# Kernel tuning notes

Measured on AMD Instinct MI355X. Metric: run time of the kernel, lower is better.

Reference implementation:

```python
import jax, jax.numpy as jnp
import numpy as np

DIM = 512
HIDDEN = 1024
H2 = HIDDEN // 2
B = 384


def setup_inputs() -> dict:
    key = jax.random.key(0)
    ks = jax.random.split(key, 10)
    s_in = 1.0 / np.sqrt(DIM)
    s_h = 1.0 / np.sqrt(H2)
    return {
        "x_samples": jax.random.normal(ks[0], (B, DIM), dtype=jnp.float32),
        "y_samples": jax.random.normal(ks[1], (B, DIM), dtype=jnp.float32),
        "w1_mu": jax.random.uniform(ks[2], (DIM, H2), jnp.float32, -s_in, s_in),
        "b1_mu": jax.random.uniform(ks[3], (H2,), jnp.float32, -s_in, s_in),
        "w2_mu": jax.random.uniform(ks[4], (H2, DIM), jnp.float32, -s_h, s_h),
        "b2_mu": jax.random.uniform(ks[5], (DIM,), jnp.float32, -s_h, s_h),
        "w1_lv": jax.random.uniform(ks[6], (DIM, H2), jnp.float32, -s_in, s_in),
        "b1_lv": jax.random.uniform(ks[7], (H2,), jnp.float32, -s_in, s_in),
        "w2_lv": jax.random.uniform(ks[8], (H2, DIM), jnp.float32, -s_h, s_h),
        "b2_lv": jax.random.uniform(ks[9], (DIM,), jnp.float32, -s_h, s_h),
    }


def reference(x_samples, y_samples, w1_mu, b1_mu, w2_mu, b2_mu,
              w1_lv, b1_lv, w2_lv, b2_lv):
    batch_size = y_samples.shape[0]
    # p_mu / p_logvar MLPs
    mu = jax.nn.relu(x_samples @ w1_mu + b1_mu) @ w2_mu + b2_mu           # [B, D]
    logvar = jnp.tanh(jax.nn.relu(x_samples @ w1_lv + b1_lv) @ w2_lv + b2_lv)  # [B, D]
    inv_var = jnp.exp(-logvar)

    # positive log-likelihood per sample
    positive = (-(mu - y_samples) ** 2 * 0.5 * inv_var - logvar * 0.5).sum(-1)  # [B]

    # pairwise Gaussian log-likelihoods: all_probs[i, j] = log N(y_j; mu_i)
    diff = y_samples[None, :, :] - mu[:, None, :]                          # [B, B, D]
    all_probs = (-diff ** 2 * 0.5 * inv_var[:, None, :]
                 - logvar[:, None, :] * 0.5).sum(-1)                       # [B, B]

    # faithful to the torch broadcast: [B,B] + [B,B,1] -> [B,B,B]
    diag_mask = jnp.eye(batch_size, dtype=jnp.float32)[:, :, None] * -20.0  # [B, B, 1]
    scores = all_probs + diag_mask                                         # [B, B, B]
    negative = jax.scipy.special.logsumexp(scores, axis=0) - jnp.log(batch_size - 1.0)  # [B, B]

    upper = (positive - negative).mean()

    loglikeli = (-(mu - y_samples) ** 2 * inv_var - logvar).sum(1).mean(0)
    return loglikeli + jax.lax.stop_gradient(-loglikeli + upper)
```

## Files before the change

kernel.cpp:

```cpp
#include <hip/hip_runtime.h>
#include <math.h>

#define DIM  512
#define H2   512
#define BSZ  384



template<bool RELU>
__device__ __forceinline__ void gemm_tile(
    const float* __restrict__ A, const float* __restrict__ B,
    const float* __restrict__ bias, float* __restrict__ C,
    int m0, int n0,
    float (*As)[34], float (*Bs)[64])
{
    const int tid = threadIdx.x;
    const int tx = tid & 15;
    const int ty = tid >> 4;

    const int r_a  = tid >> 3;
    const int kg_a = tid & 7;
    const int kr_b = tid >> 4;
    const int cg_b = tid & 15;

    float acc[2][4] = {};

    float4 a_pf  = *(const float4*)&A[(size_t)(m0 + r_a) * 512 + kg_a * 4];
    float4 b_pf0 = *(const float4*)&B[(size_t)kr_b        * 512 + n0 + cg_b * 4];
    float4 b_pf1 = *(const float4*)&B[(size_t)(kr_b + 16) * 512 + n0 + cg_b * 4];

    for (int it = 0; it < 16; ++it) {
        __syncthreads();
        {
            float av[4];
            *(float4*)av = a_pf;
            #pragma unroll
            for (int j = 0; j < 4; ++j) As[kg_a * 4 + j][r_a] = av[j];
            *(float4*)&Bs[kr_b][cg_b * 4]      = b_pf0;
            *(float4*)&Bs[kr_b + 16][cg_b * 4] = b_pf1;
        }
        __syncthreads();

        if (it < 15) {
            const int k0n = (it + 1) * 32;
            a_pf  = *(const float4*)&A[(size_t)(m0 + r_a) * 512 + k0n + kg_a * 4];
            b_pf0 = *(const float4*)&B[(size_t)(k0n + kr_b)      * 512 + n0 + cg_b * 4];
            b_pf1 = *(const float4*)&B[(size_t)(k0n + kr_b + 16) * 512 + n0 + cg_b * 4];
        }

        #pragma unroll
        for (int kk = 0; kk < 32; ++kk) {
            const float a0 = As[kk][ty * 2 + 0];
            const float a1 = As[kk][ty * 2 + 1];
            const float4 bv = *(const float4*)&Bs[kk][tx * 4];
            acc[0][0] += a0 * bv.x; acc[0][1] += a0 * bv.y;
            acc[0][2] += a0 * bv.z; acc[0][3] += a0 * bv.w;
            acc[1][0] += a1 * bv.x; acc[1][1] += a1 * bv.y;
            acc[1][2] += a1 * bv.z; acc[1][3] += a1 * bv.w;
        }
    }

    float bb[4] = {0.f, 0.f, 0.f, 0.f};
    if (RELU) *(float4*)bb = *(const float4*)&bias[n0 + tx * 4];
    #pragma unroll
    for (int i = 0; i < 2; ++i) {
        float4 o;
        if (RELU) {
            o.x = fmaxf(acc[i][0] + bb[0], 0.f);
            o.y = fmaxf(acc[i][1] + bb[1], 0.f);
            o.z = fmaxf(acc[i][2] + bb[2], 0.f);
            o.w = fmaxf(acc[i][3] + bb[3], 0.f);
        } else {
            o.x = acc[i][0]; o.y = acc[i][1]; o.z = acc[i][2]; o.w = acc[i][3];
        }
        *(float4*)&C[(size_t)(m0 + ty * 2 + i) * 512 + n0 + tx * 4] = o;
    }
}

__global__ __launch_bounds__(256) void k_layer1(
    const float* __restrict__ x,
    const float* __restrict__ w1mu, const float* __restrict__ b1mu,
    const float* __restrict__ w1lv, const float* __restrict__ b1lv,
    const float* __restrict__ y,
    float* __restrict__ hmu, float* __restrict__ hlv,
    float* __restrict__ m1p, float* __restrict__ m2p)
{
    __shared__ float As[32][34];
    __shared__ float Bs[32][64];

    const int b = blockIdx.x;
    const int tid = threadIdx.x;

    if (b >= 192) {
        __shared__ float r1[2][512];
        __shared__ float r2[2][512];
        const int sb = b - 192;
        const int c4 = tid & 127;
        const int rh = tid >> 7;
        const int r0 = sb * 64 + rh * 32;
        float s1[4] = {0.f, 0.f, 0.f, 0.f};
        float s2[4] = {0.f, 0.f, 0.f, 0.f};
        for (int r = 0; r < 32; ++r) {
            float v[4];
            *(float4*)v = *(const float4*)&y[(size_t)(r0 + r) * 512 + c4 * 4];
            #pragma unroll
            for (int j = 0; j < 4; ++j) { s1[j] += v[j]; s2[j] += v[j] * v[j]; }
        }
        #pragma unroll
        for (int j = 0; j < 4; ++j) { r1[rh][c4 * 4 + j] = s1[j]; r2[rh][c4 * 4 + j] = s2[j]; }
        __syncthreads();
        if (rh == 0) {
            float4 o1, o2;
            o1.x = s1[0] + r1[1][c4 * 4 + 0]; o1.y = s1[1] + r1[1][c4 * 4 + 1];
            o1.z = s1[2] + r1[1][c4 * 4 + 2]; o1.w = s1[3] + r1[1][c4 * 4 + 3];
            o2.x = s2[0] + r2[1][c4 * 4 + 0]; o2.y = s2[1] + r2[1][c4 * 4 + 1];
            o2.z = s2[2] + r2[1][c4 * 4 + 2]; o2.w = s2[3] + r2[1][c4 * 4 + 3];
            *(float4*)&m1p[sb * 512 + c4 * 4] = o1;
            *(float4*)&m2p[sb * 512 + c4 * 4] = o2;
        }
        return;
    }

    const int branch = b >> 7 >= 1 ? 1 : (b >= 96 ? 1 : 0);
    const int idx = branch ? b - 96 : b;
    const int m0 = (idx >> 3) * 32;
    const int n0 = (idx & 7) * 64;

    if (branch == 0)
        gemm_tile<true>(x, w1mu, b1mu, hmu, m0, n0, As, Bs);
    else
        gemm_tile<true>(x, w1lv, b1lv, hlv, m0, n0, As, Bs);
}

__global__ __launch_bounds__(256) void k_layer2(
    const float* __restrict__ hmu, const float* __restrict__ hlv,
    const float* __restrict__ w2mu, const float* __restrict__ w2lv,
    float* __restrict__ gmu, float* __restrict__ glv)
{
    __shared__ float As[32][34];
    __shared__ float Bs[32][64];

    const int b = blockIdx.x;
    const int branch = b >= 96 ? 1 : 0;
    const int idx = branch ? b - 96 : b;
    const int m0 = (idx >> 3) * 32;
    const int n0 = (idx & 7) * 64;

    if (branch == 0)
        gemm_tile<false>(hmu, w2mu, nullptr, gmu, m0, n0, As, Bs);
    else
        gemm_tile<false>(hlv, w2lv, nullptr, glv, m0, n0, As, Bs);
}

__global__ __launch_bounds__(256) void k_epilogue(
    const float* __restrict__ gmu, const float* __restrict__ glv,
    const float* __restrict__ b2mu, const float* __restrict__ b2lv,
    const float* __restrict__ y,
    const float* __restrict__ m1p, const float* __restrict__ m2p,
    double* __restrict__ partials)
{
    __shared__ double wsum[4];
    const int tid = threadIdx.x;
    const float inv_b = 1.0f / (float)BSZ;

    float tsum = 0.f;
    #pragma unroll
    for (int jj = 0; jj < 2; ++jj) {
        const int e4 = blockIdx.x * 512 + tid * 2 + jj;
        const int col4 = e4 & 127;
        const size_t off = (size_t)e4 * 4;

        float gm[4], gl[4], yv[4], bm[4], bl[4], s1[4], s2[4];
        *(float4*)gm = *(const float4*)&gmu[off];
        *(float4*)gl = *(const float4*)&glv[off];
        *(float4*)yv = *(const float4*)&y[off];
        *(float4*)bm = *(const float4*)&b2mu[col4 * 4];
        *(float4*)bl = *(const float4*)&b2lv[col4 * 4];
        #pragma unroll
        for (int j = 0; j < 4; ++j) { s1[j] = 0.f; s2[j] = 0.f; }
        #pragma unroll
        for (int t = 0; t < 6; ++t) {
            float p1[4], p2[4];
            *(float4*)p1 = *(const float4*)&m1p[t * 512 + col4 * 4];
            *(float4*)p2 = *(const float4*)&m2p[t * 512 + col4 * 4];
            #pragma unroll
            for (int j = 0; j < 4; ++j) { s1[j] += p1[j]; s2[j] += p2[j]; }
        }
        #pragma unroll
        for (int j = 0; j < 4; ++j) {
            const float m1 = s1[j] * inv_b;
            const float m2 = s2[j] * inv_b;
            const float mu = gm[j] + bm[j];
            const float lv = tanhf(gl[j] + bl[j]);
            const float iv = expf(-lv);
            tsum += iv * ((yv[j] * yv[j] - m2) + 2.f * mu * (m1 - yv[j]));
        }
    }

    float s = tsum;
    #pragma unroll
    for (int off = 32; off > 0; off >>= 1) s += __shfl_down(s, off);
    if ((tid & 63) == 0) wsum[tid >> 6] = (double)s;
    __syncthreads();
    if (tid == 0)
        partials[blockIdx.x] = wsum[0] + wsum[1] + wsum[2] + wsum[3];
}

__global__ void k_final(const double* __restrict__ partials, float* __restrict__ out)
{
    const int t = threadIdx.x;
    double v = partials[t] + (t < 32 ? partials[64 + t] : 0.0);
    #pragma unroll
    for (int off = 32; off > 0; off >>= 1) v += __shfl_down(v, off);
    if (t == 0) {
        const double C0 = 5.381602146862063e-12;
        out[0] = (float)(-0.5 * v / (double)BSZ - C0);
    }
}

extern "C" void kernel_launch(void* const* d_in, const int* in_sizes, int n_in,
                              void* d_out, int out_size, void* d_ws, size_t ws_size,
                              hipStream_t stream) {
    const float* x    = (const float*)d_in[0];
    const float* y    = (const float*)d_in[1];
    const float* w1mu = (const float*)d_in[2];
    const float* b1mu = (const float*)d_in[3];
    const float* w2mu = (const float*)d_in[4];
    const float* b2mu = (const float*)d_in[5];
    const float* w1lv = (const float*)d_in[6];
    const float* b1lv = (const float*)d_in[7];
    const float* w2lv = (const float*)d_in[8];
    const float* b2lv = (const float*)d_in[9];
    float* out = (float*)d_out;

    float* ws = (float*)d_ws;
    float* hmu = ws;
    float* hlv = ws + 196608;
    float* gmu = ws + 393216;
    float* glv = ws + 589824;
    float* m1p = ws + 786432;
    float* m2p = ws + 789504;
    double* partials = (double*)(ws + 792576);

    k_layer1<<<198, 256, 0, stream>>>(x, w1mu, b1mu, w1lv, b1lv, y,
                                      hmu, hlv, m1p, m2p);
    k_layer2<<<192, 256, 0, stream>>>(hmu, hlv, w2mu, w2lv, gmu, glv);
    k_epilogue<<<96, 256, 0, stream>>>(gmu, glv, b2mu, b2lv, y, m1p, m2p, partials);
    k_final<<<1, 64, 0, stream>>>(partials, out);
}
```

Baseline: 110.8 us.

## Fuse layer-2 GEMMs with epilogue and final reduction via last-block counter

```diff
diff --git a/kernel.cpp b/kernel.cpp
--- a/kernel.cpp
+++ b/kernel.cpp
@@ -4,7 +4,6 @@
 #define DIM  512
 #define H2   512
 #define BSZ  384
-
 
 
 template<bool RELU>
@@ -83,7 +82,8 @@
     const float* __restrict__ w1lv, const float* __restrict__ b1lv,
     const float* __restrict__ y,
     float* __restrict__ hmu, float* __restrict__ hlv,
-    float* __restrict__ m1p, float* __restrict__ m2p)
+    float* __restrict__ m1p, float* __restrict__ m2p,
+    unsigned* __restrict__ ctr)
 {
     __shared__ float As[32][34];
     __shared__ float Bs[32][64];
@@ -95,6 +95,7 @@
         __shared__ float r1[2][512];
         __shared__ float r2[2][512];
         const int sb = b - 192;
+        if (sb == 0 && tid == 0) *ctr = 0u;
         const int c4 = tid & 127;
         const int rh = tid >> 7;
         const int r0 = sb * 64 + rh * 32;
@@ -121,7 +122,7 @@
         return;
     }
 
-    const int branch = b >> 7 >= 1 ? 1 : (b >= 96 ? 1 : 0);
+    const int branch = b >= 96 ? 1 : 0;
     const int idx = branch ? b - 96 : b;
     const int m0 = (idx >> 3) * 32;
     const int n0 = (idx & 7) * 64;
@@ -132,68 +133,127 @@
         gemm_tile<true>(x, w1lv, b1lv, hlv, m0, n0, As, Bs);
 }
 
-__global__ __launch_bounds__(256) void k_layer2(
+__global__ __launch_bounds__(256) void k2_fused(
     const float* __restrict__ hmu, const float* __restrict__ hlv,
     const float* __restrict__ w2mu, const float* __restrict__ w2lv,
-    float* __restrict__ gmu, float* __restrict__ glv)
-{
-    __shared__ float As[32][34];
-    __shared__ float Bs[32][64];
-
-    const int b = blockIdx.x;
-    const int branch = b >= 96 ? 1 : 0;
-    const int idx = branch ? b - 96 : b;
-    const int m0 = (idx >> 3) * 32;
-    const int n0 = (idx & 7) * 64;
-
-    if (branch == 0)
-        gemm_tile<false>(hmu, w2mu, nullptr, gmu, m0, n0, As, Bs);
-    else
-        gemm_tile<false>(hlv, w2lv, nullptr, glv, m0, n0, As, Bs);
-}
-
-__global__ __launch_bounds__(256) void k_epilogue(
-    const float* __restrict__ gmu, const float* __restrict__ glv,
     const float* __restrict__ b2mu, const float* __restrict__ b2lv,
     const float* __restrict__ y,
     const float* __restrict__ m1p, const float* __restrict__ m2p,
-    double* __restrict__ partials)
+    double* __restrict__ partials, unsigned* __restrict__ ctr,
+    float* __restrict__ out)
 {
+    __shared__ float As[2][32][18];
+    __shared__ float Bs[2][32][64];
+    __shared__ float ivs[16][64];
     __shared__ double wsum[4];
+    __shared__ int lastFlag;
+
+    const int b   = blockIdx.x;
     const int tid = threadIdx.x;
-    const float inv_b = 1.0f / (float)BSZ;
+    const int half = tid >> 7;
+    const int t    = tid & 127;
+
+    const int m0 = (b >> 3) * 16;
+    const int n0 = (b & 7) * 64;
+
+    const float* __restrict__ A = half ? hlv : hmu;
+    const float* __restrict__ B = half ? w2lv : w2mu;
+    float (*as)[18] = As[half];
+    float (*bs)[64] = Bs[half];
+
+    const int r_a  = t >> 3;
+    const int kg_a = t & 7;
+    const int kr_b = t >> 4;
+    const int cg_b = t & 15;
+
+    const int tx = t & 15;
+    const int ty = t >> 4;
+
+    float acc[2][4] = {};
+
+    float4 a_pf = *(const float4*)&A[(size_t)(m0 + r_a) * 512 + kg_a * 4];
+    float4 b_pf[4];
+    #pragma unroll
+    for (int q = 0; q < 4; ++q)
+        b_pf[q] = *(const float4*)&B[(size_t)(kr_b + q * 8) * 512 + n0 + cg_b * 4];
+
+    for (int it = 0; it < 16; ++it) {
+        __syncthreads();
+        {
+            float av[4];
+            *(float4*)av = a_pf;
+            #pragma unroll
+            for (int j = 0; j < 4; ++j) as[kg_a * 4 + j][r_a] = av[j];
+            #pragma unroll
+            for (int q = 0; q < 4; ++q)
+                *(float4*)&bs[kr_b + q * 8][cg_b * 4] = b_pf[q];
+        }
+        __syncthreads();
+
+        if (it < 15) {
+            const int k0n = (it + 1) * 32;
+            a_pf = *(const float4*)&A[(size_t)(m0 + r_a) * 512 + k0n + kg_a * 4];
+            #pragma unroll
+            for (int q = 0; q < 4; ++q)
+                b_pf[q] = *(const float4*)&B[(size_t)(k0n + kr_b + q * 8) * 512 + n0 + cg_b * 4];
+        }
+
+        #pragma unroll
+        for (int kk = 0; kk < 32; ++kk) {
+            const float a0 = as[kk][ty * 2 + 0];
+            const float a1 = as[kk][ty * 2 + 1];
+            const float4 bv = *(const float4*)&bs[kk][tx * 4];
+            acc[0][0] += a0 * bv.x; acc[0][1] += a0 * bv.y;
+            acc[0][2] += a0 * bv.z; acc[0][3] += a0 * bv.w;
+            acc[1][0] += a1 * bv.x; acc[1][1] += a1 * bv.y;
+            acc[1][2] += a1 * bv.z; acc[1][3] += a1 * bv.w;
+        }
+    }
 
     float tsum = 0.f;
-    #pragma unroll
-    for (int jj = 0; jj < 2; ++jj) {
-        const int e4 = blockIdx.x * 512 + tid * 2 + jj;
-        const int col4 = e4 & 127;
-        const size_t off = (size_t)e4 * 4;
-
-        float gm[4], gl[4], yv[4], bm[4], bl[4], s1[4], s2[4];
-        *(float4*)gm = *(const float4*)&gmu[off];
-        *(float4*)gl = *(const float4*)&glv[off];
-        *(float4*)yv = *(const float4*)&y[off];
-        *(float4*)bm = *(const float4*)&b2mu[col4 * 4];
-        *(float4*)bl = *(const float4*)&b2lv[col4 * 4];
+    float bm[4], s1[4], s2[4], yv0[4], yv1[4];
+
+    if (half) {
+        float bl[4];
+        *(float4*)bl = *(const float4*)&b2lv[n0 + tx * 4];
+        #pragma unroll
+        for (int i = 0; i < 2; ++i) {
+            #pragma unroll
+            for (int j = 0; j < 4; ++j) {
+                const float lv = tanhf(acc[i][j] + bl[j]);
+                ivs[ty * 2 + i][tx * 4 + j] = expf(-lv);
+            }
+        }
+    } else {
+        *(float4*)bm = *(const float4*)&b2mu[n0 + tx * 4];
         #pragma unroll
         for (int j = 0; j < 4; ++j) { s1[j] = 0.f; s2[j] = 0.f; }
         #pragma unroll
-        for (int t = 0; t < 6; ++t) {
+        for (int p = 0; p < 6; ++p) {
             float p1[4], p2[4];
-            *(float4*)p1 = *(const float4*)&m1p[t * 512 + col4 * 4];
-            *(float4*)p2 = *(const float4*)&m2p[t * 512 + col4 * 4];
+            *(float4*)p1 = *(const float4*)&m1p[p * 512 + n0 + tx * 4];
+            *(float4*)p2 = *(const float4*)&m2p[p * 512 + n0 + tx * 4];
             #pragma unroll
             for (int j = 0; j < 4; ++j) { s1[j] += p1[j]; s2[j] += p2[j]; }
         }
-        #pragma unroll
-        for (int j = 0; j < 4; ++j) {
-            const float m1 = s1[j] * inv_b;
-            const float m2 = s2[j] * inv_b;
-            const float mu = gm[j] + bm[j];
-            const float lv = tanhf(gl[j] + bl[j]);
-            const float iv = expf(-lv);
-            tsum += iv * ((yv[j] * yv[j] - m2) + 2.f * mu * (m1 - yv[j]));
+        *(float4*)yv0 = *(const float4*)&y[(size_t)(m0 + ty * 2 + 0) * 512 + n0 + tx * 4];
+        *(float4*)yv1 = *(const float4*)&y[(size_t)(m0 + ty * 2 + 1) * 512 + n0 + tx * 4];
+    }
+    __syncthreads();
+
+    if (!half) {
+        const float inv_b = 1.0f / (float)BSZ;
+        #pragma unroll
+        for (int i = 0; i < 2; ++i) {
+            const float* yv = i ? yv1 : yv0;
+            #pragma unroll
+            for (int j = 0; j < 4; ++j) {
+                const float m1 = s1[j] * inv_b;
+                const float m2 = s2[j] * inv_b;
+                const float mu = acc[i][j] + bm[j];
+                const float iv = ivs[ty * 2 + i][tx * 4 + j];
+                tsum += iv * ((yv[j] * yv[j] - m2) + 2.f * mu * (m1 - yv[j]));
+            }
         }
     }
 
@@ -202,19 +262,25 @@
     for (int off = 32; off > 0; off >>= 1) s += __shfl_down(s, off);
     if ((tid & 63) == 0) wsum[tid >> 6] = (double)s;
     __syncthreads();
-    if (tid == 0)
-        partials[blockIdx.x] = wsum[0] + wsum[1] + wsum[2] + wsum[3];
-}
-
-__global__ void k_final(const double* __restrict__ partials, float* __restrict__ out)
-{
-    const int t = threadIdx.x;
-    double v = partials[t] + (t < 32 ? partials[64 + t] : 0.0);
-    #pragma unroll
-    for (int off = 32; off > 0; off >>= 1) v += __shfl_down(v, off);
-    if (t == 0) {
-        const double C0 = 5.381602146862063e-12;
-        out[0] = (float)(-0.5 * v / (double)BSZ - C0);
+    if (tid == 0) {
+        partials[b] = wsum[0] + wsum[1] + wsum[2] + wsum[3];
+        __threadfence();
+        const unsigned old = atomicAdd(ctr, 1u);
+        lastFlag = (old == 191u);
+    }
+    __syncthreads();
+
+    if (lastFlag) {
+        __threadfence();
+        if (tid < 64) {
+            double v = partials[tid] + partials[tid + 64] + partials[tid + 128];
+            #pragma unroll
+            for (int off = 32; off > 0; off >>= 1) v += __shfl_down(v, off);
+            if (tid == 0) {
+                const double C0 = 5.381602146862063e-12;
+                out[0] = (float)(-0.5 * v / (double)BSZ - C0);
+            }
+        }
     }
 }
 
@@ -236,15 +302,13 @@
     float* ws = (float*)d_ws;
     float* hmu = ws;
     float* hlv = ws + 196608;
-    float* gmu = ws + 393216;
-    float* glv = ws + 589824;
-    float* m1p = ws + 786432;
-    float* m2p = ws + 789504;
-    double* partials = (double*)(ws + 792576);
+    float* m1p = ws + 393216;
+    float* m2p = ws + 396288;
+    double* partials = (double*)(ws + 399360);
+    unsigned* ctr = (unsigned*)(ws + 399744);
 
     k_layer1<<<198, 256, 0, stream>>>(x, w1mu, b1mu, w1lv, b1lv, y,
-                                      hmu, hlv, m1p, m2p);
-    k_layer2<<<192, 256, 0, stream>>>(hmu, hlv, w2mu, w2lv, gmu, glv);
-    k_epilogue<<<96, 256, 0, stream>>>(gmu, glv, b2mu, b2lv, y, m1p, m2p, partials);
-    k_final<<<1, 64, 0, stream>>>(partials, out);
+                                      hmu, hlv, m1p, m2p, ctr);
+    k2_fused<<<192, 256, 0, stream>>>(hmu, hlv, w2mu, w2lv, b2mu, b2lv, y,
+                                      m1p, m2p, partials, ctr, out);
 }
```

Result: slower. 123.9 us (+11.8%).

## Split-K GEMM tiles across warps, double block count, fuse final reduction

Applied to the files above, without the earlier changes.

```diff
diff --git a/kernel.cpp b/kernel.cpp
--- a/kernel.cpp
+++ b/kernel.cpp
@@ -6,95 +6,122 @@
 #define BSZ  384
 
 
-
 template<bool RELU>
-__device__ __forceinline__ void gemm_tile(
+__device__ __forceinline__ void gemm_tile32(
     const float* __restrict__ A, const float* __restrict__ B,
     const float* __restrict__ bias, float* __restrict__ C,
     int m0, int n0,
-    float (*As)[34], float (*Bs)[64])
-{
-    const int tid = threadIdx.x;
-    const int tx = tid & 15;
-    const int ty = tid >> 4;
-
-    const int r_a  = tid >> 3;
-    const int kg_a = tid & 7;
-    const int kr_b = tid >> 4;
-    const int cg_b = tid & 15;
-
-    float acc[2][4] = {};
-
-    float4 a_pf  = *(const float4*)&A[(size_t)(m0 + r_a) * 512 + kg_a * 4];
-    float4 b_pf0 = *(const float4*)&B[(size_t)kr_b        * 512 + n0 + cg_b * 4];
-    float4 b_pf1 = *(const float4*)&B[(size_t)(kr_b + 16) * 512 + n0 + cg_b * 4];
-
-    for (int it = 0; it < 16; ++it) {
+    float (*As4)[32][36], float (*Bs4)[32][36], float (*Cs)[1024])
+{
+    const int tid = threadIdx.x;
+    const int w  = tid >> 6;
+    const int t  = tid & 63;
+    const int lx = t & 7;
+    const int ly = t >> 3;
+    const int kg = t & 7;
+    const int rq = t >> 3;
+    const int kbase = w * 128;
+
+    float (*as)[36] = As4[w];
+    float (*bs)[36] = Bs4[w];
+
+    float acc[4][4] = {};
+    float4 apf[4], bpf[4];
+    #pragma unroll
+    for (int q = 0; q < 4; ++q) {
+        apf[q] = *(const float4*)&A[(size_t)(m0 + rq + q * 8) * 512 + kbase + kg * 4];
+        bpf[q] = *(const float4*)&B[(size_t)(kbase + rq + q * 8) * 512 + n0 + kg * 4];
+    }
+
+    for (int it = 0; it < 4; ++it) {
         __syncthreads();
-        {
+        #pragma unroll
+        for (int q = 0; q < 4; ++q) {
             float av[4];
-            *(float4*)av = a_pf;
-            #pragma unroll
-            for (int j = 0; j < 4; ++j) As[kg_a * 4 + j][r_a] = av[j];
-            *(float4*)&Bs[kr_b][cg_b * 4]      = b_pf0;
-            *(float4*)&Bs[kr_b + 16][cg_b * 4] = b_pf1;
+            *(float4*)av = apf[q];
+            #pragma unroll
+            for (int j = 0; j < 4; ++j) as[kg * 4 + j][rq + q * 8] = av[j];
+            *(float4*)&bs[rq + q * 8][kg * 4] = bpf[q];
         }
         __syncthreads();
 
-        if (it < 15) {
-            const int k0n = (it + 1) * 32;
-            a_pf  = *(const float4*)&A[(size_t)(m0 + r_a) * 512 + k0n + kg_a * 4];
-            b_pf0 = *(const float4*)&B[(size_t)(k0n + kr_b)      * 512 + n0 + cg_b * 4];
-            b_pf1 = *(const float4*)&B[(size_t)(k0n + kr_b + 16) * 512 + n0 + cg_b * 4];
+        if (it < 3) {
+            const int k0 = kbase + (it + 1) * 32;
+            #pragma unroll
+            for (int q = 0; q < 4; ++q) {
+                apf[q] = *(const float4*)&A[(size_t)(m0 + rq + q * 8) * 512 + k0 + kg * 4];
+                bpf[q] = *(const float4*)&B[(size_t)(k0 + rq + q * 8) * 512 + n0 + kg * 4];
+            }
         }
 
         #pragma unroll
         for (int kk = 0; kk < 32; ++kk) {
-            const float a0 = As[kk][ty * 2 + 0];
-            const float a1 = As[kk][ty * 2 + 1];
-            const float4 bv = *(const float4*)&Bs[kk][tx * 4];
-            acc[0][0] += a0 * bv.x; acc[0][1] += a0 * bv.y;
-            acc[0][2] += a0 * bv.z; acc[0][3] += a0 * bv.w;
-            acc[1][0] += a1 * bv.x; acc[1][1] += a1 * bv.y;
-            acc[1][2] += a1 * bv.z; acc[1][3] += a1 * bv.w;
-        }
-    }
-
-    float bb[4] = {0.f, 0.f, 0.f, 0.f};
-    if (RELU) *(float4*)bb = *(const float4*)&bias[n0 + tx * 4];
-    #pragma unroll
-    for (int i = 0; i < 2; ++i) {
-        float4 o;
-        if (RELU) {
-            o.x = fmaxf(acc[i][0] + bb[0], 0.f);
-            o.y = fmaxf(acc[i][1] + bb[1], 0.f);
-            o.z = fmaxf(acc[i][2] + bb[2], 0.f);
-            o.w = fmaxf(acc[i][3] + bb[3], 0.f);
-        } else {
-            o.x = acc[i][0]; o.y = acc[i][1]; o.z = acc[i][2]; o.w = acc[i][3];
-        }
-        *(float4*)&C[(size_t)(m0 + ty * 2 + i) * 512 + n0 + tx * 4] = o;
-    }
-}
-
-__global__ __launch_bounds__(256) void k_layer1(
+            float av[4], bv[4];
+            *(float4*)av = *(const float4*)&as[kk][ly * 4];
+            *(float4*)bv = *(const float4*)&bs[kk][lx * 4];
+            #pragma unroll
+            for (int i = 0; i < 4; ++i)
+                #pragma unroll
+                for (int j = 0; j < 4; ++j)
+                    acc[i][j] += av[i] * bv[j];
+        }
+    }
+
+    if (w) {
+        #pragma unroll
+        for (int i = 0; i < 4; ++i)
+            *(float4*)&Cs[w - 1][(ly * 4 + i) * 32 + lx * 4] = *(const float4*)&acc[i][0];
+    }
+    __syncthreads();
+    if (!w) {
+        #pragma unroll
+        for (int q = 0; q < 3; ++q)
+            #pragma unroll
+            for (int i = 0; i < 4; ++i) {
+                float cv[4];
+                *(float4*)cv = *(const float4*)&Cs[q][(ly * 4 + i) * 32 + lx * 4];
+                #pragma unroll
+                for (int j = 0; j < 4; ++j) acc[i][j] += cv[j];
+            }
+        float bb[4] = {0.f, 0.f, 0.f, 0.f};
+        if (RELU) *(float4*)bb = *(const float4*)&bias[n0 + lx * 4];
+        #pragma unroll
+        for (int i = 0; i < 4; ++i) {
+            float4 o;
+            if (RELU) {
+                o.x = fmaxf(acc[i][0] + bb[0], 0.f);
+                o.y = fmaxf(acc[i][1] + bb[1], 0.f);
+                o.z = fmaxf(acc[i][2] + bb[2], 0.f);
+                o.w = fmaxf(acc[i][3] + bb[3], 0.f);
+            } else {
+                o.x = acc[i][0]; o.y = acc[i][1]; o.z = acc[i][2]; o.w = acc[i][3];
+            }
+            *(float4*)&C[(size_t)(m0 + ly * 4 + i) * 512 + n0 + lx * 4] = o;
+        }
+    }
+}
+
+__global__ __launch_bounds__(256) void k_l1(
     const float* __restrict__ x,
     const float* __restrict__ w1mu, const float* __restrict__ b1mu,
     const float* __restrict__ w1lv, const float* __restrict__ b1lv,
     const float* __restrict__ y,
     float* __restrict__ hmu, float* __restrict__ hlv,
-    float* __restrict__ m1p, float* __restrict__ m2p)
-{
-    __shared__ float As[32][34];
-    __shared__ float Bs[32][64];
+    float* __restrict__ m1p, float* __restrict__ m2p,
+    unsigned* __restrict__ ctr)
+{
+    __shared__ float As[4][32][36];
+    __shared__ float Bs[4][32][36];
+    __shared__ float Cs[3][1024];
 
     const int b = blockIdx.x;
     const int tid = threadIdx.x;
 
-    if (b >= 192) {
+    if (b >= 384) {
         __shared__ float r1[2][512];
         __shared__ float r2[2][512];
-        const int sb = b - 192;
+        const int sb = b - 384;
+        if (sb == 0 && tid == 0) *ctr = 0u;
         const int c4 = tid & 127;
         const int rh = tid >> 7;
         const int r0 = sb * 64 + rh * 32;
@@ -121,80 +148,84 @@
         return;
     }
 
-    const int branch = b >> 7 >= 1 ? 1 : (b >= 96 ? 1 : 0);
-    const int idx = branch ? b - 96 : b;
-    const int m0 = (idx >> 3) * 32;
-    const int n0 = (idx & 7) * 64;
-
-    if (branch == 0)
-        gemm_tile<true>(x, w1mu, b1mu, hmu, m0, n0, As, Bs);
+    const int branch = b >= 192;
+    const int idx = branch ? b - 192 : b;
+    const int m0 = (idx >> 4) * 32;
+    const int n0 = (idx & 15) * 32;
+
+    if (!branch)
+        gemm_tile32<true>(x, w1mu, b1mu, hmu, m0, n0, As, Bs, Cs);
     else
-        gemm_tile<true>(x, w1lv, b1lv, hlv, m0, n0, As, Bs);
-}
-
-__global__ __launch_bounds__(256) void k_layer2(
+        gemm_tile32<true>(x, w1lv, b1lv, hlv, m0, n0, As, Bs, Cs);
+}
+
+__global__ __launch_bounds__(256) void k_l2(
     const float* __restrict__ hmu, const float* __restrict__ hlv,
     const float* __restrict__ w2mu, const float* __restrict__ w2lv,
-    float* __restrict__ gmu, float* __restrict__ glv)
-{
-    __shared__ float As[32][34];
-    __shared__ float Bs[32][64];
+    float* __restrict__ gmu, float* __restrict__ glv,
+    const float* __restrict__ m1p, const float* __restrict__ m2p,
+    float* __restrict__ m1f, float* __restrict__ m2f)
+{
+    __shared__ float As[4][32][36];
+    __shared__ float Bs[4][32][36];
+    __shared__ float Cs[3][1024];
 
     const int b = blockIdx.x;
-    const int branch = b >= 96 ? 1 : 0;
-    const int idx = branch ? b - 96 : b;
-    const int m0 = (idx >> 3) * 32;
-    const int n0 = (idx & 7) * 64;
-
-    if (branch == 0)
-        gemm_tile<false>(hmu, w2mu, nullptr, gmu, m0, n0, As, Bs);
+    const int tid = threadIdx.x;
+
+    if (b >= 384) {
+        const float inv_b = 1.0f / (float)BSZ;
+        for (int c = tid; c < 512; c += 256) {
+            float s1 = 0.f, s2 = 0.f;
+            #pragma unroll
+            for (int p = 0; p < 6; ++p) { s1 += m1p[p * 512 + c]; s2 += m2p[p * 512 + c]; }
+            m1f[c] = s1 * inv_b;
+            m2f[c] = s2 * inv_b;
+        }
+        return;
+    }
+
+    const int branch = b >= 192;
+    const int idx = branch ? b - 192 : b;
+    const int m0 = (idx >> 4) * 32;
+    const int n0 = (idx & 15) * 32;
+
+    if (!branch)
+        gemm_tile32<false>(hmu, w2mu, nullptr, gmu, m0, n0, As, Bs, Cs);
     else
-        gemm_tile<false>(hlv, w2lv, nullptr, glv, m0, n0, As, Bs);
-}
-
-__global__ __launch_bounds__(256) void k_epilogue(
+        gemm_tile32<false>(hlv, w2lv, nullptr, glv, m0, n0, As, Bs, Cs);
+}
+
+__global__ __launch_bounds__(256) void k_epi(
     const float* __restrict__ gmu, const float* __restrict__ glv,
     const float* __restrict__ b2mu, const float* __restrict__ b2lv,
     const float* __restrict__ y,
-    const float* __restrict__ m1p, const float* __restrict__ m2p,
-    double* __restrict__ partials)
+    const float* __restrict__ m1f, const float* __restrict__ m2f,
+    double* __restrict__ partials, unsigned* __restrict__ ctr,
+    float* __restrict__ out)
 {
     __shared__ double wsum[4];
-    const int tid = threadIdx.x;
-    const float inv_b = 1.0f / (float)BSZ;
+    __shared__ int lastFlag;
+    const int tid = threadIdx.x;
+    const int e4 = blockIdx.x * 256 + tid;
+    const int col4 = e4 & 127;
+
+    float gm[4], gl[4], yv[4], bm[4], bl[4], v1[4], v2[4];
+    *(float4*)gm = *(const float4*)&gmu[(size_t)e4 * 4];
+    *(float4*)gl = *(const float4*)&glv[(size_t)e4 * 4];
+    *(float4*)yv = *(const float4*)&y[(size_t)e4 * 4];
+    *(float4*)bm = *(const float4*)&b2mu[col4 * 4];
+    *(float4*)bl = *(const float4*)&b2lv[col4 * 4];
+    *(float4*)v1 = *(const float4*)&m1f[col4 * 4];
+    *(float4*)v2 = *(const float4*)&m2f[col4 * 4];
 
     float tsum = 0.f;
     #pragma unroll
-    for (int jj = 0; jj < 2; ++jj) {
-        const int e4 = blockIdx.x * 512 + tid * 2 + jj;
-        const int col4 = e4 & 127;
-        const size_t off = (size_t)e4 * 4;
-
-        float gm[4], gl[4], yv[4], bm[4], bl[4], s1[4], s2[4];
-        *(float4*)gm = *(const float4*)&gmu[off];
-        *(float4*)gl = *(const float4*)&glv[off];
-        *(float4*)yv = *(const float4*)&y[off];
-        *(float4*)bm = *(const float4*)&b2mu[col4 * 4];
-        *(float4*)bl = *(const float4*)&b2lv[col4 * 4];
-        #pragma unroll
-        for (int j = 0; j < 4; ++j) { s1[j] = 0.f; s2[j] = 0.f; }
-        #pragma unroll
-        for (int t = 0; t < 6; ++t) {
-            float p1[4], p2[4];
-            *(float4*)p1 = *(const float4*)&m1p[t * 512 + col4 * 4];
-            *(float4*)p2 = *(const float4*)&m2p[t * 512 + col4 * 4];
-            #pragma unroll
-            for (int j = 0; j < 4; ++j) { s1[j] += p1[j]; s2[j] += p2[j]; }
-        }
-        #pragma unroll
-        for (int j = 0; j < 4; ++j) {
-            const float m1 = s1[j] * inv_b;
-            const float m2 = s2[j] * inv_b;
-            const float mu = gm[j] + bm[j];
-            const float lv = tanhf(gl[j] + bl[j]);
-            const float iv = expf(-lv);
-            tsum += iv * ((yv[j] * yv[j] - m2) + 2.f * mu * (m1 - yv[j]));
-        }
+    for (int j = 0; j < 4; ++j) {
+        const float mu = gm[j] + bm[j];
+        const float lv = tanhf(gl[j] + bl[j]);
+        const float iv = expf(-lv);
+        tsum += iv * ((yv[j] * yv[j] - v2[j]) + 2.f * mu * (v1[j] - yv[j]));
     }
 
     float s = tsum;
@@ -202,19 +233,24 @@
     for (int off = 32; off > 0; off >>= 1) s += __shfl_down(s, off);
     if ((tid & 63) == 0) wsum[tid >> 6] = (double)s;
     __syncthreads();
-    if (tid == 0)
+    if (tid == 0) {
         partials[blockIdx.x] = wsum[0] + wsum[1] + wsum[2] + wsum[3];
-}
-
-__global__ void k_final(const double* __restrict__ partials, float* __restrict__ out)
-{
-    const int t = threadIdx.x;
-    double v = partials[t] + (t < 32 ? partials[64 + t] : 0.0);
-    #pragma unroll
-    for (int off = 32; off > 0; off >>= 1) v += __shfl_down(v, off);
-    if (t == 0) {
-        const double C0 = 5.381602146862063e-12;
-        out[0] = (float)(-0.5 * v / (double)BSZ - C0);
+        __threadfence();
+        lastFlag = (atomicAdd(ctr, 1u) == 191u);
+    }
+    __syncthreads();
+
+    if (lastFlag) {
+        __threadfence();
+        if (tid < 64) {
+            double v = partials[tid] + partials[tid + 64] + partials[tid + 128];
+            #pragma unroll
+            for (int off = 32; off > 0; off >>= 1) v += __shfl_down(v, off);
+            if (tid == 0) {
+                const double C0 = 5.381602146862063e-12;
+                out[0] = (float)(-0.5 * v / (double)BSZ - C0);
+            }
+        }
     }
 }
 
@@ -240,11 +276,15 @@
     float* glv = ws + 589824;
     float* m1p = ws + 786432;
     float* m2p = ws + 789504;
-    double* partials = (double*)(ws + 792576);
-
-    k_layer1<<<198, 256, 0, stream>>>(x, w1mu, b1mu, w1lv, b1lv, y,
-                                      hmu, hlv, m1p, m2p);
-    k_layer2<<<192, 256, 0, stream>>>(hmu, hlv, w2mu, w2lv, gmu, glv);
-    k_epilogue<<<96, 256, 0, stream>>>(gmu, glv, b2mu, b2lv, y, m1p, m2p, partials);
-    k_final<<<1, 64, 0, stream>>>(partials, out);
-}
+    float* m1f = ws + 792576;
+    float* m2f = ws + 793088;
+    double* partials = (double*)(ws + 793600);
+    unsigned* ctr = (unsigned*)(ws + 793984);
+
+    k_l1<<<390, 256, 0, stream>>>(x, w1mu, b1mu, w1lv, b1lv, y,
+                                  hmu, hlv, m1p, m2p, ctr);
+    k_l2<<<385, 256, 0, stream>>>(hmu, hlv, w2mu, w2lv, gmu, glv,
+                                  m1p, m2p, m1f, m2f);
+    k_epi<<<192, 256, 0, stream>>>(gmu, glv, b2mu, b2lv, y,
+                                   m1f, m2f, partials, ctr, out);
+}
```

New measurement: 116.4 us. 1.05x slower.

## Fuse layer-2 GEMM, epilogue and final reduction with inter-block atomic sync

Applied to the files above, without the earlier changes.

```diff
diff --git a/kernel.cpp b/kernel.cpp
--- a/kernel.cpp
+++ b/kernel.cpp
@@ -4,7 +4,6 @@
 #define DIM  512
 #define H2   512
 #define BSZ  384
-
 
 
 template<bool RELU>
@@ -83,7 +82,8 @@
     const float* __restrict__ w1lv, const float* __restrict__ b1lv,
     const float* __restrict__ y,
     float* __restrict__ hmu, float* __restrict__ hlv,
-    float* __restrict__ m1p, float* __restrict__ m2p)
+    float* __restrict__ m1p, float* __restrict__ m2p,
+    unsigned* __restrict__ sync_)
 {
     __shared__ float As[32][34];
     __shared__ float Bs[32][64];
@@ -95,6 +95,7 @@
         __shared__ float r1[2][512];
         __shared__ float r2[2][512];
         const int sb = b - 192;
+        if (sb == 0 && tid < 97) sync_[tid] = 0u;
         const int c4 = tid & 127;
         const int rh = tid >> 7;
         const int r0 = sb * 64 + rh * 32;
@@ -121,7 +122,7 @@
         return;
     }
 
-    const int branch = b >> 7 >= 1 ? 1 : (b >= 96 ? 1 : 0);
+    const int branch = b >= 96 ? 1 : 0;
     const int idx = branch ? b - 96 : b;
     const int m0 = (idx >> 3) * 32;
     const int n0 = (idx & 7) * 64;
@@ -132,15 +133,23 @@
         gemm_tile<true>(x, w1lv, b1lv, hlv, m0, n0, As, Bs);
 }
 
-__global__ __launch_bounds__(256) void k_layer2(
+__global__ __launch_bounds__(256) void k2_fused(
     const float* __restrict__ hmu, const float* __restrict__ hlv,
     const float* __restrict__ w2mu, const float* __restrict__ w2lv,
-    float* __restrict__ gmu, float* __restrict__ glv)
+    const float* __restrict__ b2mu, const float* __restrict__ b2lv,
+    const float* __restrict__ y,
+    const float* __restrict__ m1p, const float* __restrict__ m2p,
+    float* __restrict__ gmu, float* __restrict__ glv,
+    double* __restrict__ partials, unsigned* __restrict__ sync_,
+    float* __restrict__ out)
 {
     __shared__ float As[32][34];
     __shared__ float Bs[32][64];
-
-    const int b = blockIdx.x;
+    __shared__ double wsum[4];
+    __shared__ int lastFlag;
+
+    const int b   = blockIdx.x;
+    const int tid = threadIdx.x;
     const int branch = b >= 96 ? 1 : 0;
     const int idx = branch ? b - 96 : b;
     const int m0 = (idx >> 3) * 32;
@@ -150,71 +159,75 @@
         gemm_tile<false>(hmu, w2mu, nullptr, gmu, m0, n0, As, Bs);
     else
         gemm_tile<false>(hlv, w2lv, nullptr, glv, m0, n0, As, Bs);
-}
-
-__global__ __launch_bounds__(256) void k_epilogue(
-    const float* __restrict__ gmu, const float* __restrict__ glv,
-    const float* __restrict__ b2mu, const float* __restrict__ b2lv,
-    const float* __restrict__ y,
-    const float* __restrict__ m1p, const float* __restrict__ m2p,
-    double* __restrict__ partials)
-{
-    __shared__ double wsum[4];
-    const int tid = threadIdx.x;
+
+    unsigned* pc = sync_ + 1 + idx;
+    __syncthreads();
+    if (tid == 0) {
+        __threadfence();
+        atomicAdd(pc, 1u);
+        while (atomicAdd(pc, 0u) < 2u) __builtin_amdgcn_s_sleep(2);
+    }
+    __syncthreads();
+    __threadfence();
+
+    const int r  = tid >> 4;
+    const int c4 = tid & 15;
+    const int row = m0 + branch * 16 + r;
+    const int col = n0 + c4 * 4;
+    const size_t off = (size_t)row * 512 + col;
+
+    float gm[4], gl[4], yv[4], bm[4], bl[4], s1[4], s2[4];
+    *(float4*)gm = *(const float4*)&gmu[off];
+    *(float4*)gl = *(const float4*)&glv[off];
+    *(float4*)yv = *(const float4*)&y[off];
+    *(float4*)bm = *(const float4*)&b2mu[col];
+    *(float4*)bl = *(const float4*)&b2lv[col];
+    #pragma unroll
+    for (int j = 0; j < 4; ++j) { s1[j] = 0.f; s2[j] = 0.f; }
+    #pragma unroll
+    for (int p = 0; p < 6; ++p) {
+        float p1[4], p2[4];
+        *(float4*)p1 = *(const float4*)&m1p[p * 512 + col];
+        *(float4*)p2 = *(const float4*)&m2p[p * 512 + col];
+        #pragma unroll
+        for (int j = 0; j < 4; ++j) { s1[j] += p1[j]; s2[j] += p2[j]; }
+    }
+
     const float inv_b = 1.0f / (float)BSZ;
-
     float tsum = 0.f;
     #pragma unroll
-    for (int jj = 0; jj < 2; ++jj) {
-        const int e4 = blockIdx.x * 512 + tid * 2 + jj;
-        const int col4 = e4 & 127;
-        const size_t off = (size_t)e4 * 4;
-
-        float gm[4], gl[4], yv[4], bm[4], bl[4], s1[4], s2[4];
-        *(float4*)gm = *(const float4*)&gmu[off];
-        *(float4*)gl = *(const float4*)&glv[off];
-        *(float4*)yv = *(const float4*)&y[off];
-        *(float4*)bm = *(const float4*)&b2mu[col4 * 4];
-        *(float4*)bl = *(const float4*)&b2lv[col4 * 4];
-        #pragma unroll
-        for (int j = 0; j < 4; ++j) { s1[j] = 0.f; s2[j] = 0.f; }
-        #pragma unroll
-        for (int t = 0; t < 6; ++t) {
-            float p1[4], p2[4];
-            *(float4*)p1 = *(const float4*)&m1p[t * 512 + col4 * 4];
-            *(float4*)p2 = *(const float4*)&m2p[t * 512 + col4 * 4];
+    for (int j = 0; j < 4; ++j) {
+        const float m1 = s1[j] * inv_b;
+        const float m2 = s2[j] * inv_b;
+        const float mu = gm[j] + bm[j];
+        const float lv = tanhf(gl[j] + bl[j]);
+        const float iv = expf(-lv);
+        tsum += iv * ((yv[j] * yv[j] - m2) + 2.f * mu * (m1 - yv[j]));
+    }
+
+    float s = tsum;
+    #pragma unroll
+    for (int o = 32; o > 0; o >>= 1) s += __shfl_down(s, o);
+    if ((tid & 63) == 0) wsum[tid >> 6] = (double)s;
+    __syncthreads();
+    if (tid == 0) {
+        partials[b] = wsum[0] + wsum[1] + wsum[2] + wsum[3];
+        __threadfence();
+        lastFlag = (atomicAdd(&sync_[0], 1u) == 191u);
+    }
+    __syncthreads();
+
+    if (lastFlag) {
+        __threadfence();
+        if (tid < 64) {
+            double v = partials[tid] + partials[tid + 64] + partials[tid + 128];
             #pragma unroll
-            for (int j = 0; j < 4; ++j) { s1[j] += p1[j]; s2[j] += p2[j]; }
-        }
-        #pragma unroll
-        for (int j = 0; j < 4; ++j) {
-            const float m1 = s1[j] * inv_b;
-            const float m2 = s2[j] * inv_b;
-            const float mu = gm[j] + bm[j];
-            const float lv = tanhf(gl[j] + bl[j]);
-            const float iv = expf(-lv);
-            tsum += iv * ((yv[j] * yv[j] - m2) + 2.f * mu * (m1 - yv[j]));
-        }
-    }
-
-    float s = tsum;
-    #pragma unroll
-    for (int off = 32; off > 0; off >>= 1) s += __shfl_down(s, off);
-    if ((tid & 63) == 0) wsum[tid >> 6] = (double)s;
-    __syncthreads();
-    if (tid == 0)
-        partials[blockIdx.x] = wsum[0] + wsum[1] + wsum[2] + wsum[3];
-}
-
-__global__ void k_final(const double* __restrict__ partials, float* __restrict__ out)
-{
-    const int t = threadIdx.x;
-    double v = partials[t] + (t < 32 ? partials[64 + t] : 0.0);
-    #pragma unroll
-    for (int off = 32; off > 0; off >>= 1) v += __shfl_down(v, off);
-    if (t == 0) {
-        const double C0 = 5.381602146862063e-12;
-        out[0] = (float)(-0.5 * v / (double)BSZ - C0);
+            for (int o = 32; o > 0; o >>= 1) v += __shfl_down(v, o);
+            if (tid == 0) {
+                const double C0 = 5.381602146862063e-12;
+                out[0] = (float)(-0.5 * v / (double)BSZ - C0);
+            }
+        }
     }
 }
 
@@ -240,11 +253,11 @@
     float* glv = ws + 589824;
     float* m1p = ws + 786432;
     float* m2p = ws + 789504;
-    double* partials = (double*)(ws + 792576);
+    double* partials = (double*)(ws + 793600);
+    unsigned* sync_ = (unsigned*)(ws + 793984);
 
     k_layer1<<<198, 256, 0, stream>>>(x, w1mu, b1mu, w1lv, b1lv, y,
-                                      hmu, hlv, m1p, m2p);
-    k_layer2<<<192, 256, 0, stream>>>(hmu, hlv, w2mu, w2lv, gmu, glv);
-    k_epilogue<<<96, 256, 0, stream>>>(gmu, glv, b2mu, b2lv, y, m1p, m2p, partials);
-    k_final<<<1, 64, 0, stream>>>(partials, out);
-}
+                                      hmu, hlv, m1p, m2p, sync_);
+    k2_fused<<<192, 256, 0, stream>>>(hmu, hlv, w2mu, w2lv, b2mu, b2lv, y,
+                                      m1p, m2p, gmu, glv, partials, sync_, out);
+}
```

Result: slower. 127.3 us (+14.8%).
